# Optimization experiments

Measured on AMD Instinct MI355X. Metric: run time of the kernel, lower is better.

## Reference

```python
import jax, jax.numpy as jnp
import numpy as np

B = 16      # graphs
NPG = 1024  # nodes per graph (equal-sized, contiguous)
N = B * NPG
K = 12      # knn neighbors
DM = 128    # d_model
DH = 256    # d_hidden = 2*d_model
L = 3       # num_layers
DI = 2 * DM + 4  # msg mlp input dim


def _mlp2(x, W1, b1, W2, b2):
    return jax.nn.silu(x @ W1 + b1) @ W2 + b2


def setup_inputs() -> dict:
    key = jax.random.key(0)
    ks = list(jax.random.split(key, 16))
    def nrm(k, shape, fan):
        return jax.random.normal(k, shape, jnp.float32) / np.float32(np.sqrt(fan))
    return dict(
        x=jax.random.normal(ks[0], (N, 3), jnp.float32),
        batch=(jnp.arange(N) // NPG).astype(jnp.int32),
        in_W1=nrm(ks[1], (3, DM), 3), in_b1=jnp.zeros((DM,), jnp.float32),
        in_W2=nrm(ks[2], (DM, DM), DM), in_b2=jnp.zeros((DM,), jnp.float32),
        msg_W1=nrm(ks[3], (L, DI, DH), DI), msg_b1=jnp.zeros((L, DH), jnp.float32),
        msg_W2=nrm(ks[4], (L, DH, DM), DH), msg_b2=jnp.zeros((L, DM), jnp.float32),
        upd_W1=nrm(ks[5], (L, 2 * DM, DH), 2 * DM), upd_b1=jnp.zeros((L, DH), jnp.float32),
        upd_W2=nrm(ks[6], (L, DH, DM), DH), upd_b2=jnp.zeros((L, DM), jnp.float32),
        norm_w=jnp.ones((L, DM), jnp.float32), norm_b=jnp.zeros((L, DM), jnp.float32),
        norm_ms=jnp.ones((L, DM), jnp.float32),
        gate_W1=nrm(ks[7], (DM, DM), DM), gate_b1=jnp.zeros((DM,), jnp.float32),
        gate_W2=nrm(ks[8], (DM, 1), DM), gate_b2=jnp.zeros((1,), jnp.float32),
        head_W1=nrm(ks[9], (DM, DM), DM), head_b1=jnp.zeros((DM,), jnp.float32),
        head_W2=nrm(ks[10], (DM, 1), DM), head_b2=jnp.zeros((1,), jnp.float32),
    )


def _knn_edges(pos):
    # pos: [N,2]; graphs are contiguous blocks of NPG nodes -> blocked knn
    p3 = pos.reshape(B, NPG, 2)
    d2 = jnp.sum((p3[:, :, None, :] - p3[:, None, :, :]) ** 2, axis=-1)  # [B,n,n]
    d2 = jnp.where(jnp.eye(NPG, dtype=bool)[None], jnp.inf, d2)          # no self loops
    idx = jax.lax.top_k(-d2, K)[1]  # [B,n,K] nearest neighbors (sources)
    offs = (jnp.arange(B) * NPG)[:, None, None]
    src = (idx + offs).reshape(-1)
    dst = jnp.broadcast_to(jnp.arange(N).reshape(B, NPG, 1), (B, NPG, K)).reshape(-1)
    return src, dst


def _graph_norm(h, batch, cnt, w, b, ms):
    # PyG GraphNorm: out = w * (h - ms*mean) / sqrt(var + eps) + b, per-graph stats
    mean = jax.ops.segment_sum(h, batch, B) / cnt
    out = h - mean[batch] * ms
    var = jax.ops.segment_sum(out ** 2, batch, B) / cnt
    return w * out / jnp.sqrt(var + 1e-5)[batch] + b


def _forward(x, batch, in_W1, in_b1, in_W2, in_b2, msg_W1, msg_b1, msg_W2, msg_b2,
             upd_W1, upd_b1, upd_W2, upd_b2, norm_w, norm_b, norm_ms,
             gate_W1, gate_b1, gate_W2, gate_b2, head_W1, head_b1, head_W2, head_b2):
    pos = x[:, 1:3]
    src, dst = _knn_edges(pos)
    # edge_attr = [dx, dy, dist, ds]
    dp = pos[src] - pos[dst]
    dist = jnp.sqrt(jnp.sum(dp ** 2, axis=-1, keepdims=True) + 1e-12)
    ds = x[src, 0:1] - x[dst, 0:1]
    ea = jnp.concatenate([dp, dist, ds], axis=-1)  # [E,4]

    h = _mlp2(x, in_W1, in_b1, in_W2, in_b2)       # [N,DM]
    cnt = jax.ops.segment_sum(jnp.ones((N,), h.dtype), batch, B)[:, None]

    for i in range(L):
        m_in = jnp.concatenate([h[dst], h[src], ea], axis=-1)       # [E,2*DM+4]
        m = _mlp2(m_in, msg_W1[i], msg_b1[i], msg_W2[i], msg_b2[i])  # [E,DM]
        agg = jax.ops.segment_sum(m, dst, N)                         # scatter_add
        dh = _mlp2(jnp.concatenate([h, agg], axis=-1),
                   upd_W1[i], upd_b1[i], upd_W2[i], upd_b2[i])
        h = h + dh  # dropout is identity at inference
        h = _graph_norm(h, batch, cnt, norm_w[i], norm_b[i], norm_ms[i])

    # gated attention pool: segment softmax over gate logits
    gl = (jnp.tanh(h @ gate_W1 + gate_b1) @ gate_W2 + gate_b2)[:, 0]  # [N]
    gmax = jax.ops.segment_max(gl, batch, B)
    e = jnp.exp(gl - gmax[batch])
    a = e / jax.ops.segment_sum(e, batch, B)[batch]
    pooled = jax.ops.segment_sum(h * a[:, None], batch, B)            # [B,DM]

    return _mlp2(pooled, head_W1, head_b1, head_W2, head_b2)[:, 0]    # [B]


def reference(x, batch, in_W1, in_b1, in_W2, in_b2, msg_W1, msg_b1, msg_W2, msg_b2,
              upd_W1, upd_b1, upd_W2, upd_b2, norm_w, norm_b, norm_ms,
              gate_W1, gate_b1, gate_W2, gate_b2, head_W1, head_b1, head_W2, head_b2):
    return _forward(x, batch, in_W1, in_b1, in_W2, in_b2, msg_W1, msg_b1, msg_W2, msg_b2,
                    upd_W1, upd_b1, upd_W2, upd_b2, norm_w, norm_b, norm_ms,
                    gate_W1, gate_b1, gate_W2, gate_b2, head_W1, head_b1, head_W2, head_b2)
```

## Files before the change

### kernel.cpp

```cpp
#include <hip/hip_runtime.h>
#include <math.h>

#define NPTS 16384
#define BGR 16
#define NPGR 1024
#define KNN 12
#define DM 128
#define DH 256
#define NL 3
#define EDG (NPTS*KNN)

typedef unsigned short u16;
typedef unsigned int u32;
typedef __attribute__((ext_vector_type(8))) short short8;
typedef __attribute__((ext_vector_type(4))) float floatx4;

__device__ __forceinline__ float silu_f(float x) {
    return x / (1.0f + __expf(-x));
}
__device__ __forceinline__ u16 f2bf(float f) {
    union { float f; u32 u; } v; v.f = f;
    u32 r = v.u + 0x7fffu + ((v.u >> 16) & 1u);
    return (u16)(r >> 16);
}
__device__ __forceinline__ float bf2f(u16 b) {
    union { u32 u; float f; } v; v.u = ((u32)b) << 16;
    return v.f;
}

#define KPPB 16
#define PSTR 209
__global__ __launch_bounds__(256) void knn_kernel(const float* __restrict__ x,
                                                  int* __restrict__ srcb,
                                                  float* __restrict__ ea) {
#pragma clang fp contract(off)
    __shared__ float2 pxy[NPGR];
    __shared__ float s0[NPGR];
    __shared__ float sdf[KPPB * PSTR];
    __shared__ int   sif[KPPB * PSTR];
    __shared__ int   sel[KPPB][KNN];
    int t = threadIdx.x;
    int g   = blockIdx.x / (NPGR / KPPB);
    int blk = blockIdx.x % (NPGR / KPPB);
    int base = g * NPGR;
    for (int j = t; j < NPGR; j += 256) {
        const float* xp = x + (size_t)(base + j) * 3;
        s0[j] = xp[0];
        pxy[j] = make_float2(xp[1], xp[2]);
    }
    __syncthreads();
    int r  = t & 15;
    int pt = t >> 4;
    int il = blk * KPPB + pt;
    float2 pil = pxy[il];
    float xi = pil.x, yi = pil.y;
    float nd[KNN]; int ni[KNN];
#pragma unroll
    for (int k = 0; k < KNN; ++k) { nd[k] = 3.4e38f; ni[k] = 0x7fffffff; }
    for (int jj = 0; jj < 64; ++jj) {
        int j = jj * 16 + r;
        if (j == il) continue;
        float2 p = pxy[j];
        float dx = p.x - xi;
        float dy = p.y - yi;
        float dx2 = dx * dx;
        float dy2 = dy * dy;
        float d2 = dx2 + dy2;
        if (d2 < nd[KNN-1]) {
            float cd = d2; int ci = j;
#pragma unroll
            for (int k = 0; k < KNN; ++k) {
                bool sw = cd < nd[k];
                float tdv = sw ? nd[k] : cd;
                nd[k] = sw ? cd : nd[k];
                cd = tdv;
                int tiv = sw ? ni[k] : ci;
                ni[k] = sw ? ci : ni[k];
                ci = tiv;
            }
        }
    }
#pragma unroll
    for (int k = 0; k < KNN; ++k) {
        sdf[pt * PSTR + r * 13 + k] = nd[k];
        sif[pt * PSTR + r * 13 + k] = ni[k];
    }
    __syncthreads();
    if (r == 0) {
        int head[16];
#pragma unroll
        for (int q = 0; q < 16; ++q) head[q] = 0;
#pragma unroll
        for (int k = 0; k < KNN; ++k) {
            float bd = 3.4e38f; int bi = 0x7fffffff; int bq = 0;
#pragma unroll
            for (int q = 0; q < 16; ++q) {
                int hq = head[q];
                float d = (hq < KNN) ? sdf[pt * PSTR + q * 13 + hq] : 3.4e38f;
                int  ix = (hq < KNN) ? sif[pt * PSTR + q * 13 + hq] : 0x7fffffff;
                if (d < bd || (d == bd && ix < bi)) { bd = d; bi = ix; bq = q; }
            }
            head[bq]++;
            sel[pt][k] = bi;
        }
    }
    __syncthreads();
    if (r < KNN) {
        int k = r;
        int j = sel[pt][k];
        size_t e = (size_t)(base + il) * KNN + k;
        srcb[e] = base + j;
        float x0i = s0[il];
        float2 pj = pxy[j];
        float dpx = pj.x - xi, dpy = pj.y - yi;
        float a = dpx * dpx;
        float b = dpy * dpy;
        float dist = sqrtf(a + b + 1e-12f);
        float dsv = s0[j] - x0i;
        *(float4*)(ea + e * 4) = make_float4(dpx, dpy, dist, dsv);
    }
}

__global__ __launch_bounds__(128) void in_mlp_kernel(const float* __restrict__ x,
    const float* __restrict__ W1, const float* __restrict__ b1,
    const float* __restrict__ W2, const float* __restrict__ b2,
    float* __restrict__ h, u16* __restrict__ hh, u16* __restrict__ hl) {
    __shared__ float hid[8][DM];
    __shared__ float xl[8][3];
    int t = threadIdx.x;
    int nb = blockIdx.x * 8;
    if (t < 24) xl[t / 3][t % 3] = x[(size_t)nb * 3 + t];
    __syncthreads();
    float w0 = W1[t], w1 = W1[DM + t], w2 = W1[2 * DM + t], bb = b1[t];
#pragma unroll
    for (int gi = 0; gi < 8; ++gi) {
        float v = xl[gi][0] * w0 + xl[gi][1] * w1 + xl[gi][2] * w2 + bb;
        hid[gi][t] = silu_f(v);
    }
    __syncthreads();
    float acc[8];
    float b2v = b2[t];
#pragma unroll
    for (int gi = 0; gi < 8; ++gi) acc[gi] = b2v;
    for (int k = 0; k < DM; ++k) {
        float w = W2[k * DM + t];
#pragma unroll
        for (int gi = 0; gi < 8; ++gi) acc[gi] += hid[gi][k] * w;
    }
#pragma unroll
    for (int gi = 0; gi < 8; ++gi) {
        size_t idx = (size_t)(nb + gi) * DM + t;
        float v = acc[gi];
        h[idx] = v;
        u16 hi = f2bf(v);
        hh[idx] = hi;
        hl[idx] = f2bf(v - bf2f(hi));
    }
}

#define MBM 64
#define MBN 128
#define MBK 32
#define MLDA 40

__global__ __launch_bounds__(256) void mgemm_kernel(
    const u16* __restrict__ A0h, const u16* __restrict__ A0l, int k0, int lda0,
    const u16* __restrict__ A1h, const u16* __restrict__ A1l, int lda1,
    const u16* __restrict__ Wh, const u16* __restrict__ Wl, int K,
    const float* __restrict__ bias, int biasN,
    const float* __restrict__ resid, int ldres,
    float* __restrict__ outf, u16* __restrict__ outh, u16* __restrict__ outl, int ldout,
    int act)
{
    __shared__ __align__(16) u16 Ash[MBM * MLDA];
    __shared__ __align__(16) u16 Asl[MBM * MLDA];
    __shared__ __align__(16) u16 Bsh[MBN * MLDA];
    __shared__ __align__(16) u16 Bsl[MBN * MLDA];
    int t = threadIdx.x;
    int row0 = blockIdx.x * MBM, col0 = blockIdx.y * MBN;
    int lane = t & 63, w = t >> 6;
    int wm = (w >> 1) * 32, wn = (w & 1) * 64;
    int quad = lane >> 4, r15 = lane & 15;
    int arow = t >> 2, acol = (t & 3) * 8;
    int brow = t >> 1, bcol = (t & 1) * 16;

    floatx4 acc[2][4];
#pragma unroll
    for (int m = 0; m < 2; ++m)
#pragma unroll
        for (int n = 0; n < 4; ++n) acc[m][n] = (floatx4){0.f, 0.f, 0.f, 0.f};

    for (int kt = 0; kt < K; kt += MBK) {
        const u16 *Aph, *Apl;
        if (kt < k0) {
            Aph = A0h + (size_t)(row0 + arow) * lda0 + kt + acol;
            Apl = A0l + (size_t)(row0 + arow) * lda0 + kt + acol;
        } else {
            Aph = A1h + (size_t)(row0 + arow) * lda1 + (kt - k0) + acol;
            Apl = A1l + (size_t)(row0 + arow) * lda1 + (kt - k0) + acol;
        }
        uint4 avh = *(const uint4*)Aph;
        uint4 avl = *(const uint4*)Apl;
        const u16* Bph = Wh + (size_t)(col0 + brow) * K + kt + bcol;
        const u16* Bpl = Wl + (size_t)(col0 + brow) * K + kt + bcol;
        uint4 bh0 = ((const uint4*)Bph)[0];
        uint4 bh1 = ((const uint4*)Bph)[1];
        uint4 bl0 = ((const uint4*)Bpl)[0];
        uint4 bl1 = ((const uint4*)Bpl)[1];
        __syncthreads();
        *(uint4*)(Ash + arow * MLDA + acol) = avh;
        *(uint4*)(Asl + arow * MLDA + acol) = avl;
        uint4* bdh = (uint4*)(Bsh + brow * MLDA + bcol);
        uint4* bdl = (uint4*)(Bsl + brow * MLDA + bcol);
        bdh[0] = bh0; bdh[1] = bh1;
        bdl[0] = bl0; bdl[1] = bl1;
        __syncthreads();
        short8 ah[2], alo[2], bhf[4], blf[4];
#pragma unroll
        for (int m = 0; m < 2; ++m) {
            ah[m]  = *(const short8*)(Ash + (wm + m*16 + r15) * MLDA + quad*8);
            alo[m] = *(const short8*)(Asl + (wm + m*16 + r15) * MLDA + quad*8);
        }
#pragma unroll
        for (int n = 0; n < 4; ++n) {
            bhf[n] = *(const short8*)(Bsh + (wn + n*16 + r15) * MLDA + quad*8);
            blf[n] = *(const short8*)(Bsl + (wn + n*16 + r15) * MLDA + quad*8);
        }
#pragma unroll
        for (int m = 0; m < 2; ++m)
#pragma unroll
            for (int n = 0; n < 4; ++n) {
                acc[m][n] = __builtin_amdgcn_mfma_f32_16x16x32_bf16(ah[m],  bhf[n], acc[m][n], 0, 0, 0);
                acc[m][n] = __builtin_amdgcn_mfma_f32_16x16x32_bf16(ah[m],  blf[n], acc[m][n], 0, 0, 0);
                acc[m][n] = __builtin_amdgcn_mfma_f32_16x16x32_bf16(alo[m], bhf[n], acc[m][n], 0, 0, 0);
            }
    }
#pragma unroll
    for (int n = 0; n < 4; ++n) {
        int col = col0 + wn + n*16 + r15;
        float bv = (bias && col < biasN) ? bias[col] : 0.f;
#pragma unroll
        for (int m = 0; m < 2; ++m) {
#pragma unroll
            for (int reg = 0; reg < 4; ++reg) {
                int row = row0 + wm + m*16 + quad*4 + reg;
                float v = acc[m][n][reg] + bv;
                if (act == 1) v = silu_f(v);
                else if (act == 2) v = tanhf(v);
                if (resid) v += resid[(size_t)row * ldres + col];
                size_t oidx = (size_t)row * ldout + col;
                if (outf) outf[oidx] = v;
                if (outh) {
                    u16 hi = f2bf(v);
                    outh[oidx] = hi;
                    outl[oidx] = f2bf(v - bf2f(hi));
                }
            }
        }
    }
}

#define M2BM 128
__global__ __launch_bounds__(256) void mgemm128_kernel(
    const u16* __restrict__ A0h, const u16* __restrict__ A0l, int k0, int lda0,
    const u16* __restrict__ A1h, const u16* __restrict__ A1l, int lda1,
    const u16* __restrict__ Wh, const u16* __restrict__ Wl, int K,
    const float* __restrict__ bias, int biasN,
    float* __restrict__ outf, u16* __restrict__ outh, u16* __restrict__ outl, int ldout,
    int act)
{
    __shared__ __align__(16) u16 Ash[M2BM * MLDA];
    __shared__ __align__(16) u16 Asl[M2BM * MLDA];
    __shared__ __align__(16) u16 Bsh[MBN * MLDA];
    __shared__ __align__(16) u16 Bsl[MBN * MLDA];
    int t = threadIdx.x;
    int row0 = blockIdx.x * M2BM, col0 = blockIdx.y * MBN;
    int lane = t & 63, w = t >> 6;
    int wm = (w >> 1) * 64, wn = (w & 1) * 64;
    int quad = lane >> 4, r15 = lane & 15;
    int srow = t >> 1, scol = (t & 1) * 16;

    floatx4 acc[4][4];
#pragma unroll
    for (int m = 0; m < 4; ++m)
#pragma unroll
        for (int n = 0; n < 4; ++n) acc[m][n] = (floatx4){0.f, 0.f, 0.f, 0.f};

    for (int kt = 0; kt < K; kt += MBK) {
        const u16 *Aph, *Apl;
        if (kt < k0) {
            Aph = A0h + (size_t)(row0 + srow) * lda0 + kt + scol;
            Apl = A0l + (size_t)(row0 + srow) * lda0 + kt + scol;
        } else {
            Aph = A1h + (size_t)(row0 + srow) * lda1 + (kt - k0) + scol;
            Apl = A1l + (size_t)(row0 + srow) * lda1 + (kt - k0) + scol;
        }
        uint4 avh0 = ((const uint4*)Aph)[0];
        uint4 avh1 = ((const uint4*)Aph)[1];
        uint4 avl0 = ((const uint4*)Apl)[0];
        uint4 avl1 = ((const uint4*)Apl)[1];
        const u16* Bph = Wh + (size_t)(col0 + srow) * K + kt + scol;
        const u16* Bpl = Wl + (size_t)(col0 + srow) * K + kt + scol;
        uint4 bh0 = ((const uint4*)Bph)[0];
        uint4 bh1 = ((const uint4*)Bph)[1];
        uint4 bl0 = ((const uint4*)Bpl)[0];
        uint4 bl1 = ((const uint4*)Bpl)[1];
        __syncthreads();
        uint4* adh = (uint4*)(Ash + srow * MLDA + scol);
        uint4* adl = (uint4*)(Asl + srow * MLDA + scol);
        adh[0] = avh0; adh[1] = avh1;
        adl[0] = avl0; adl[1] = avl1;
        uint4* bdh = (uint4*)(Bsh + srow * MLDA + scol);
        uint4* bdl = (uint4*)(Bsl + srow * MLDA + scol);
        bdh[0] = bh0; bdh[1] = bh1;
        bdl[0] = bl0; bdl[1] = bl1;
        __syncthreads();
        short8 ah[4], alo[4], bhf[4], blf[4];
#pragma unroll
        for (int m = 0; m < 4; ++m) {
            ah[m]  = *(const short8*)(Ash + (wm + m*16 + r15) * MLDA + quad*8);
            alo[m] = *(const short8*)(Asl + (wm + m*16 + r15) * MLDA + quad*8);
        }
#pragma unroll
        for (int n = 0; n < 4; ++n) {
            bhf[n] = *(const short8*)(Bsh + (wn + n*16 + r15) * MLDA + quad*8);
            blf[n] = *(const short8*)(Bsl + (wn + n*16 + r15) * MLDA + quad*8);
        }
#pragma unroll
        for (int m = 0; m < 4; ++m)
#pragma unroll
            for (int n = 0; n < 4; ++n) {
                acc[m][n] = __builtin_amdgcn_mfma_f32_16x16x32_bf16(ah[m],  bhf[n], acc[m][n], 0, 0, 0);
                acc[m][n] = __builtin_amdgcn_mfma_f32_16x16x32_bf16(ah[m],  blf[n], acc[m][n], 0, 0, 0);
                acc[m][n] = __builtin_amdgcn_mfma_f32_16x16x32_bf16(alo[m], bhf[n], acc[m][n], 0, 0, 0);
            }
    }
#pragma unroll
    for (int n = 0; n < 4; ++n) {
        int col = col0 + wn + n*16 + r15;
        float bv = (bias && col < biasN) ? bias[col] : 0.f;
#pragma unroll
        for (int m = 0; m < 4; ++m) {
#pragma unroll
            for (int reg = 0; reg < 4; ++reg) {
                int row = row0 + wm + m*16 + quad*4 + reg;
                float v = acc[m][n][reg] + bv;
                if (act == 1) v = silu_f(v);
                size_t oidx = (size_t)row * ldout + col;
                if (outf) outf[oidx] = v;
                if (outh) {
                    u16 hi = f2bf(v);
                    outh[oidx] = hi;
                    outl[oidx] = f2bf(v - bf2f(hi));
                }
            }
        }
    }
}

__global__ __launch_bounds__(256) void edge_agg_kernel(
    const float* __restrict__ CS,
    const int* __restrict__ srcb, const float* __restrict__ ea,
    const float* __restrict__ W1ea,
    u16* __restrict__ HSh, u16* __restrict__ HSl)
{
    int i = blockIdx.x, t = threadIdx.x;
    __shared__ int ss[KNN];
    __shared__ float sea[KNN * 4];
    if (t < KNN) ss[t] = srcb[(size_t)i * KNN + t];
    if (t < KNN * 4) sea[t] = ea[(size_t)i * KNN * 4 + t];
    __syncthreads();
    float base = CS[(size_t)i * 512 + t];
    float wa = W1ea[t], wb = W1ea[DH + t], wc = W1ea[2 * DH + t], wd = W1ea[3 * DH + t];
    float hs = 0.f;
#pragma unroll
    for (int e = 0; e < KNN; ++e) {
        float v = base + CS[(size_t)ss[e] * 512 + 256 + t]
                + sea[e * 4 + 0] * wa + sea[e * 4 + 1] * wb
                + sea[e * 4 + 2] * wc + sea[e * 4 + 3] * wd;
        hs += silu_f(v);
    }
    size_t oidx = (size_t)i * DH + t;
    u16 hi = f2bf(hs);
    HSh[oidx] = hi;
    HSl[oidx] = f2bf(hs - bf2f(hi));
}

__global__ __launch_bounds__(256) void norm_part_kernel(const float* __restrict__ hn,
                                                        float* __restrict__ psum)
{
    int g = blockIdx.x, blk = blockIdx.y;
    int t = threadIdx.x, d = t & 127, half = t >> 7;
    size_t base = ((size_t)g * NPGR + (size_t)blk * 128 + half * 64) * DM;
    float s = 0.f, s2 = 0.f;
    for (int n = 0; n < 64; ++n) {
        float v = hn[base + (size_t)n * DM + d];
        s += v; s2 += v * v;
    }
    __shared__ float ps[2][DM], ps2[2][DM];
    ps[half][d] = s; ps2[half][d] = s2;
    __syncthreads();
    if (t < DM) {
        psum[(((size_t)g * 8 + blk) * 2 + 0) * DM + d] = ps[0][d] + ps[1][d];
        psum[(((size_t)g * 8 + blk) * 2 + 1) * DM + d] = ps2[0][d] + ps2[1][d];
    }
}

__global__ __launch_bounds__(256) void norm_apply_kernel(const float* __restrict__ hn,
    float* __restrict__ h, u16* __restrict__ hh, u16* __restrict__ hl,
    const float* __restrict__ psum,
    const float* __restrict__ w, const float* __restrict__ b, const float* __restrict__ ms)
{
    int g = blockIdx.x, blk = blockIdx.y, t = threadIdx.x;
    __shared__ float mmv[DM], rst[DM], wv[DM], bv[DM];
    if (t < DM) {
        float sum = 0.f, sq = 0.f;
        for (int q = 0; q < 8; ++q) {
            sum += psum[(((size_t)g * 8 + q) * 2 + 0) * DM + t];
            sq  += psum[(((size_t)g * 8 + q) * 2 + 1) * DM + t];
        }
        float mean = sum * (1.0f / NPGR);
        float mm = mean * ms[t];
        float var = sq * (1.0f / NPGR) - 2.f * mm * mean + mm * mm;
        mmv[t] = mm;
        rst[t] = 1.0f / sqrtf(var + 1e-5f);
        wv[t] = w[t]; bv[t] = b[t];
    }
    __syncthreads();
    size_t base = ((size_t)g * NPGR + (size_t)blk * 128) * DM;
    for (int i = t; i < 128 * DM; i += 256) {
        int dd = i & 127;
        float v = hn[base + i];
        float o = wv[dd] * (v - mmv[dd]) * rst[dd] + bv[dd];
        h[base + i] = o;
        u16 hi = f2bf(o);
        hh[base + i] = hi;
        hl[base + i] = f2bf(o - bf2f(hi));
    }
}

__global__ __launch_bounds__(256) void gate_dot_kernel(const float* __restrict__ Gh,
    const float* __restrict__ gW2, const float* __restrict__ gb2,
    float* __restrict__ gl)
{
    int t = threadIdx.x, lane = t & 63, w = t >> 6;
    int node = blockIdx.x * 4 + w;
    const float* gp = Gh + (size_t)node * DM;
    float v = gp[lane] * gW2[lane] + gp[lane + 64] * gW2[lane + 64];
    for (int off = 32; off > 0; off >>= 1) v += __shfl_down(v, off, 64);
    if (lane == 0) gl[node] = v + gb2[0];
}

__global__ __launch_bounds__(256) void pool_stats_kernel(const float* __restrict__ gl,
                                                         float* __restrict__ gstat)
{
    int g = blockIdx.x, t = threadIdx.x, lane = t & 63, w = t >> 6;
    __shared__ float red[4];
    const float* gp = gl + (size_t)g * NPGR;
    float mx = -3.4e38f;
    for (int n = t; n < NPGR; n += 256) mx = fmaxf(mx, gp[n]);
    for (int off = 32; off > 0; off >>= 1) mx = fmaxf(mx, __shfl_down(mx, off, 64));
    if (lane == 0) red[w] = mx;
    __syncthreads();
    float gmax = fmaxf(fmaxf(red[0], red[1]), fmaxf(red[2], red[3]));
    __syncthreads();
    float se = 0.f;
    for (int n = t; n < NPGR; n += 256) se += __expf(gp[n] - gmax);
    for (int off = 32; off > 0; off >>= 1) se += __shfl_down(se, off, 64);
    if (lane == 0) red[w] = se;
    __syncthreads();
    if (t == 0) { gstat[g * 2] = gmax; gstat[g * 2 + 1] = red[0] + red[1] + red[2] + red[3]; }
}

__global__ __launch_bounds__(256) void pool_part_kernel(const float* __restrict__ h,
    const float* __restrict__ gl, const float* __restrict__ gstat,
    float* __restrict__ ppool)
{
    int g = blockIdx.x, blk = blockIdx.y;
    int t = threadIdx.x, d = t & 127, half = t >> 7;
    float gmax = gstat[g * 2];
    size_t nbase = (size_t)g * NPGR + (size_t)blk * 128 + half * 64;
    float p = 0.f;
    for (int n = 0; n < 64; ++n)
        p += __expf(gl[nbase + n] - gmax) * h[(nbase + n) * DM + d];
    __shared__ float ps[2][DM];
    ps[half][d] = p;
    __syncthreads();
    if (t < DM) ppool[((size_t)g * 8 + blk) * DM + d] = ps[0][d] + ps[1][d];
}

__global__ __launch_bounds__(128) void pool_head_kernel(const float* __restrict__ ppool,
    const float* __restrict__ gstat,
    const float* __restrict__ hW1, const float* __restrict__ hb1,
    const float* __restrict__ hW2, const float* __restrict__ hb2,
    float* __restrict__ outp)
{
    int g = blockIdx.x, t = threadIdx.x;
    __shared__ float pl[DM];
    __shared__ float red[2];
    float ssum = gstat[g * 2 + 1];
    float p = 0.f;
    for (int q = 0; q < 8; ++q) p += ppool[((size_t)g * 8 + q) * DM + t];
    pl[t] = p / ssum;
    __syncthreads();
    float a = hb1[t];
    for (int k = 0; k < DM; ++k) a += pl[k] * hW1[k * DM + t];
    a = silu_f(a);
    float vv = a * hW2[t];
    int lane = t & 63, w = t >> 6;
    for (int off = 32; off > 0; off >>= 1) vv += __shfl_down(vv, off, 64);
    if (lane == 0) red[w] = vv;
    __syncthreads();
    if (t == 0) outp[g] = red[0] + red[1] + hb2[0];
}

__global__ __launch_bounds__(256) void precompute_kernel(
    const float* __restrict__ msgW2, const float* __restrict__ msgb2,
    const float* __restrict__ updW1, const float* __restrict__ updb1,
    float* __restrict__ W2U, float* __restrict__ bias2)
{
    int bid = blockIdx.x; int t = threadIdx.x;
    if (bid < NL * DH) {
        int l = bid / DH, k = bid % DH;
        const float* w2row = msgW2 + (size_t)l * DH * DM + (size_t)k * DM;
        const float* u1 = updW1 + (size_t)l * 2 * DM * DH;
        float acc = 0.f;
        for (int j = 0; j < DM; ++j) acc += w2row[j] * u1[(size_t)(DM + j) * DH + t];
        W2U[(size_t)l * DH * DH + (size_t)k * DH + t] = acc;
    } else {
        int l = bid - NL * DH;
        const float* u1 = updW1 + (size_t)l * 2 * DM * DH;
        const float* b2 = msgb2 + (size_t)l * DM;
        float acc = updb1[(size_t)l * DH + t];
        for (int j = 0; j < DM; ++j) acc += 12.0f * b2[j] * u1[(size_t)(DM + j) * DH + t];
        bias2[(size_t)l * DH + t] = acc;
    }
}

struct WJob { const float* src; u16* dh; u16* dl; int K, N, ldd, off; };
struct WJobs { WJob j[16]; };
__global__ __launch_bounds__(256) void wprep_kernel(WJobs jobs) {
    WJob jb = jobs.j[blockIdx.y];
    int n = blockIdx.x;
    if (n >= jb.N) return;
    for (int k = threadIdx.x; k < jb.K; k += 256) {
        float v = jb.src[(size_t)k * jb.N + n];
        u16 hi = f2bf(v);
        u16 lo = f2bf(v - bf2f(hi));
        jb.dh[(size_t)n * jb.ldd + jb.off + k] = hi;
        jb.dl[(size_t)n * jb.ldd + jb.off + k] = lo;
    }
}

extern "C" void kernel_launch(void* const* d_in, const int* in_sizes, int n_in,
                              void* d_out, int out_size, void* d_ws, size_t ws_size,
                              hipStream_t stream) {
    const float* x     = (const float*)d_in[0];
    const float* inW1  = (const float*)d_in[2];
    const float* inb1  = (const float*)d_in[3];
    const float* inW2  = (const float*)d_in[4];
    const float* inb2  = (const float*)d_in[5];
    const float* msgW1 = (const float*)d_in[6];
    const float* msgb1 = (const float*)d_in[7];
    const float* msgW2 = (const float*)d_in[8];
    const float* msgb2 = (const float*)d_in[9];
    const float* updW1 = (const float*)d_in[10];
    const float* updb1 = (const float*)d_in[11];
    const float* updW2 = (const float*)d_in[12];
    const float* updb2 = (const float*)d_in[13];
    const float* nw    = (const float*)d_in[14];
    const float* nb    = (const float*)d_in[15];
    const float* nms   = (const float*)d_in[16];
    const float* gW1   = (const float*)d_in[17];
    const float* gb1   = (const float*)d_in[18];
    const float* gW2   = (const float*)d_in[19];
    const float* gb2   = (const float*)d_in[20];
    const float* hW1   = (const float*)d_in[21];
    const float* hb1   = (const float*)d_in[22];
    const float* hW2   = (const float*)d_in[23];
    const float* hb2   = (const float*)d_in[24];
    float* outp = (float*)d_out;

    float* ws    = (float*)d_ws;
    float* h     = ws;
    float* CSb   = h + (size_t)NPTS * DM;
    float* hnb   = CSb + (size_t)NPTS * 512;
    float* W2U   = hnb + (size_t)NPTS * DM;
    float* bias2 = W2U + (size_t)NL * DH * DH;
    float* glb   = bias2 + NL * DH;
    int*   srcb  = (int*)(glb + NPTS);
    float* eab   = (float*)(srcb + EDG);
    float* psum  = eab + (size_t)EDG * 4;
    float* gstat = psum + 16 * 8 * 2 * DM;
    float* ppool = gstat + 32;
    u16* hh  = (u16*)(ppool + 16 * 8 * DM);
    u16* hl  = hh + (size_t)NPTS * DM;
    u16* HSh = hl + (size_t)NPTS * DM;
    u16* HSl = HSh + (size_t)NPTS * DH;
    u16* Th  = HSl + (size_t)NPTS * DH;
    u16* Tl  = Th + (size_t)NPTS * DH;
    u16* WCSh = Tl + (size_t)NPTS * DH;              u16* WCSl = WCSh + (size_t)NL * 512 * DM;
    u16* WTh = WCSl + (size_t)NL * 512 * DM;         u16* WTl = WTh + (size_t)NL * DH * 384;
    u16* WUh = WTl + (size_t)NL * DH * 384;          u16* WUl = WUh + (size_t)NL * DM * DH;
    u16* WGh = WUl + (size_t)NL * DM * DH;           u16* WGl = WGh + (size_t)DM * DM;

    hipLaunchKernelGGL(precompute_kernel, dim3(NL * DH + NL), dim3(DH), 0, stream,
                       msgW2, msgb2, updW1, updb1, W2U, bias2);

    WJobs jobs;
    int ji = 0;
    for (int l = 0; l < NL; ++l) {
        jobs.j[ji++] = WJob{ msgW1 + (size_t)l * 260 * DH,            WCSh + (size_t)l * 512 * DM,            WCSl + (size_t)l * 512 * DM,            128, 256, 128, 0 };
        jobs.j[ji++] = WJob{ msgW1 + (size_t)l * 260 * DH + 128 * DH, WCSh + (size_t)l * 512 * DM + 256 * DM, WCSl + (size_t)l * 512 * DM + 256 * DM, 128, 256, 128, 0 };
        jobs.j[ji++] = WJob{ updW1 + (size_t)l * 256 * DH,            WTh + (size_t)l * DH * 384, WTl + (size_t)l * DH * 384, 128, 256, 384, 0 };
        jobs.j[ji++] = WJob{ W2U   + (size_t)l * DH * DH,             WTh + (size_t)l * DH * 384, WTl + (size_t)l * DH * 384, 256, 256, 384, 128 };
        jobs.j[ji++] = WJob{ updW2 + (size_t)l * DH * DM,             WUh + (size_t)l * DM * DH, WUl + (size_t)l * DM * DH, 256, 128, 256, 0 };
    }
    jobs.j[ji++] = WJob{ gW1, WGh, WGl, 128, 128, 128, 0 };
    hipLaunchKernelGGL(wprep_kernel, dim3(256, 16), dim3(256), 0, stream, jobs);

    hipLaunchKernelGGL(knn_kernel, dim3(NPTS / KPPB), dim3(256), 0, stream, x, srcb, eab);
    hipLaunchKernelGGL(in_mlp_kernel, dim3(NPTS / 8), dim3(128), 0, stream,
                       x, inW1, inb1, inW2, inb2, h, hh, hl);

    for (int l = 0; l < NL; ++l) {
        const float* W1l = msgW1 + (size_t)l * 260 * DH;
        hipLaunchKernelGGL(mgemm128_kernel, dim3(NPTS / M2BM, 512 / MBN), dim3(256), 0, stream,
            hh, hl, DM, DM, (const u16*)nullptr, (const u16*)nullptr, 0,
            WCSh + (size_t)l * 512 * DM, WCSl + (size_t)l * 512 * DM, DM,
            msgb1 + (size_t)l * DH, 256,
            CSb, (u16*)nullptr, (u16*)nullptr, 512, 0);
        hipLaunchKernelGGL(edge_agg_kernel, dim3(NPTS), dim3(DH), 0, stream,
            CSb, srcb, eab, W1l + (size_t)2 * DM * DH, HSh, HSl);
        hipLaunchKernelGGL(mgemm128_kernel, dim3(NPTS / M2BM, DH / MBN), dim3(256), 0, stream,
            hh, hl, DM, DM, HSh, HSl, DH,
            WTh + (size_t)l * DH * 384, WTl + (size_t)l * DH * 384, 384,
            bias2 + (size_t)l * DH, DH,
            (float*)nullptr, Th, Tl, DH, 1);
        hipLaunchKernelGGL(mgemm_kernel, dim3(NPTS / MBM, DM / MBN), dim3(256), 0, stream,
            Th, Tl, DH, DH, (const u16*)nullptr, (const u16*)nullptr, 0,
            WUh + (size_t)l * DM * DH, WUl + (size_t)l * DM * DH, DH,
            updb2 + (size_t)l * DM, DM, h, DM,
            hnb, (u16*)nullptr, (u16*)nullptr, DM, 0);
        hipLaunchKernelGGL(norm_part_kernel, dim3(BGR, 8), dim3(256), 0, stream, hnb, psum);
        hipLaunchKernelGGL(norm_apply_kernel, dim3(BGR, 8), dim3(256), 0, stream,
            hnb, h, hh, hl, psum, nw + (size_t)l * DM, nb + (size_t)l * DM, nms + (size_t)l * DM);
    }

    hipLaunchKernelGGL(mgemm_kernel, dim3(NPTS / MBM, DM / MBN), dim3(256), 0, stream,
        hh, hl, DM, DM, (const u16*)nullptr, (const u16*)nullptr, 0,
        WGh, WGl, DM, gb1, DM, (const float*)nullptr, 0,
        hnb, (u16*)nullptr, (u16*)nullptr, DM, 2);
    hipLaunchKernelGGL(gate_dot_kernel, dim3(NPTS / 4), dim3(256), 0, stream,
        hnb, gW2, gb2, glb);

    hipLaunchKernelGGL(pool_stats_kernel, dim3(BGR), dim3(256), 0, stream, glb, gstat);
    hipLaunchKernelGGL(pool_part_kernel, dim3(BGR, 8), dim3(256), 0, stream, h, glb, gstat, ppool);
    hipLaunchKernelGGL(pool_head_kernel, dim3(BGR), dim3(128), 0, stream,
        ppool, gstat, hW1, hb1, hW2, hb2, outp);
}
```

Measured before the change: 566.4 us.

## Load GEMM tiles via direct global-to-LDS with XOR swizzle; retune knn split

Both bf16 split GEMM kernels now stage A and B tiles with global_load_lds (direct global-to-LDS DMA) instead of register round-trips. The padded LDS stride is replaced by an XOR-swizzled 32-wide layout to avoid bank conflicts. The knn kernel handles 32 points per block with 8 scanning threads per point instead of 16, which halves the merge width. One update GEMM switches from the 128-row to the 64-row tile variant, increasing the block count. Correctness of the swizzle and the implicit lane-to-LDS mapping of global_load_lds is a risk.

```diff
diff --git a/kernel.cpp b/kernel.cpp
--- a/kernel.cpp
+++ b/kernel.cpp
@@ -27,17 +27,24 @@
     union { u32 u; float f; } v; v.u = ((u32)b) << 16;
     return v.f;
 }
-
-#define KPPB 16
-#define PSTR 209
+__device__ __forceinline__ void glds16(const u16* gp, u16* lp) {
+    __builtin_amdgcn_global_load_lds(
+        (const __attribute__((address_space(1))) void*)gp,
+        (__attribute__((address_space(3))) void*)lp, 16, 0, 0);
+}
+__device__ __forceinline__ int lofs(int row, int q) {
+    return row * 32 + ((q ^ ((row >> 2) & 3)) << 3);
+}
+
+#define KPPB 32
 __global__ __launch_bounds__(256) void knn_kernel(const float* __restrict__ x,
                                                   int* __restrict__ srcb,
                                                   float* __restrict__ ea) {
 #pragma clang fp contract(off)
     __shared__ float2 pxy[NPGR];
     __shared__ float s0[NPGR];
-    __shared__ float sdf[KPPB * PSTR];
-    __shared__ int   sif[KPPB * PSTR];
+    __shared__ float sdf[256 * 13];
+    __shared__ int   sif[256 * 13];
     __shared__ int   sel[KPPB][KNN];
     int t = threadIdx.x;
     int g   = blockIdx.x / (NPGR / KPPB);
@@ -49,16 +56,16 @@
         pxy[j] = make_float2(xp[1], xp[2]);
     }
     __syncthreads();
-    int r  = t & 15;
-    int pt = t >> 4;
+    int r  = t & 7;
+    int pt = t >> 3;
     int il = blk * KPPB + pt;
     float2 pil = pxy[il];
     float xi = pil.x, yi = pil.y;
     float nd[KNN]; int ni[KNN];
 #pragma unroll
     for (int k = 0; k < KNN; ++k) { nd[k] = 3.4e38f; ni[k] = 0x7fffffff; }
-    for (int jj = 0; jj < 64; ++jj) {
-        int j = jj * 16 + r;
+    for (int jj = 0; jj < 128; ++jj) {
+        int j = jj * 8 + r;
         if (j == il) continue;
         float2 p = pxy[j];
         float dx = p.x - xi;
@@ -80,24 +87,25 @@
             }
         }
     }
+    int li = pt * 8 + r;
 #pragma unroll
     for (int k = 0; k < KNN; ++k) {
-        sdf[pt * PSTR + r * 13 + k] = nd[k];
-        sif[pt * PSTR + r * 13 + k] = ni[k];
+        sdf[li * 13 + k] = nd[k];
+        sif[li * 13 + k] = ni[k];
     }
     __syncthreads();
     if (r == 0) {
-        int head[16];
-#pragma unroll
-        for (int q = 0; q < 16; ++q) head[q] = 0;
+        int head[8];
+#pragma unroll
+        for (int q = 0; q < 8; ++q) head[q] = 0;
 #pragma unroll
         for (int k = 0; k < KNN; ++k) {
             float bd = 3.4e38f; int bi = 0x7fffffff; int bq = 0;
 #pragma unroll
-            for (int q = 0; q < 16; ++q) {
+            for (int q = 0; q < 8; ++q) {
                 int hq = head[q];
-                float d = (hq < KNN) ? sdf[pt * PSTR + q * 13 + hq] : 3.4e38f;
-                int  ix = (hq < KNN) ? sif[pt * PSTR + q * 13 + hq] : 0x7fffffff;
+                float d = (hq < KNN) ? sdf[(pt * 8 + q) * 13 + hq] : 3.4e38f;
+                int  ix = (hq < KNN) ? sif[(pt * 8 + q) * 13 + hq] : 0x7fffffff;
                 if (d < bd || (d == bd && ix < bi)) { bd = d; bi = ix; bq = q; }
             }
             head[bq]++;
@@ -105,12 +113,11 @@
         }
     }
     __syncthreads();
-    if (r < KNN) {
-        int k = r;
+    float x0i = s0[il];
+    for (int k = r; k < KNN; k += 8) {
         int j = sel[pt][k];
         size_t e = (size_t)(base + il) * KNN + k;
         srcb[e] = base + j;
-        float x0i = s0[il];
         float2 pj = pxy[j];
         float dpx = pj.x - xi, dpy = pj.y - yi;
         float a = dpx * dpx;
@@ -161,7 +168,6 @@
 #define MBM 64
 #define MBN 128
 #define MBK 32
-#define MLDA 40
 
 __global__ __launch_bounds__(256) void mgemm_kernel(
     const u16* __restrict__ A0h, const u16* __restrict__ A0l, int k0, int lda0,
@@ -172,17 +178,16 @@
     float* __restrict__ outf, u16* __restrict__ outh, u16* __restrict__ outl, int ldout,
     int act)
 {
-    __shared__ __align__(16) u16 Ash[MBM * MLDA];
-    __shared__ __align__(16) u16 Asl[MBM * MLDA];
-    __shared__ __align__(16) u16 Bsh[MBN * MLDA];
-    __shared__ __align__(16) u16 Bsl[MBN * MLDA];
+    __shared__ __align__(16) u16 Ash[MBM * 32];
+    __shared__ __align__(16) u16 Asl[MBM * 32];
+    __shared__ __align__(16) u16 Bsh[MBN * 32];
+    __shared__ __align__(16) u16 Bsl[MBN * 32];
     int t = threadIdx.x;
     int row0 = blockIdx.x * MBM, col0 = blockIdx.y * MBN;
     int lane = t & 63, w = t >> 6;
     int wm = (w >> 1) * 32, wn = (w & 1) * 64;
     int quad = lane >> 4, r15 = lane & 15;
-    int arow = t >> 2, acol = (t & 3) * 8;
-    int brow = t >> 1, bcol = (t & 1) * 16;
+    int rowl = lane >> 2, slot = lane & 3;
 
     floatx4 acc[2][4];
 #pragma unroll
@@ -191,40 +196,40 @@
         for (int n = 0; n < 4; ++n) acc[m][n] = (floatx4){0.f, 0.f, 0.f, 0.f};
 
     for (int kt = 0; kt < K; kt += MBK) {
-        const u16 *Aph, *Apl;
-        if (kt < k0) {
-            Aph = A0h + (size_t)(row0 + arow) * lda0 + kt + acol;
-            Apl = A0l + (size_t)(row0 + arow) * lda0 + kt + acol;
-        } else {
-            Aph = A1h + (size_t)(row0 + arow) * lda1 + (kt - k0) + acol;
-            Apl = A1l + (size_t)(row0 + arow) * lda1 + (kt - k0) + acol;
-        }
-        uint4 avh = *(const uint4*)Aph;
-        uint4 avl = *(const uint4*)Apl;
-        const u16* Bph = Wh + (size_t)(col0 + brow) * K + kt + bcol;
-        const u16* Bpl = Wl + (size_t)(col0 + brow) * K + kt + bcol;
-        uint4 bh0 = ((const uint4*)Bph)[0];
-        uint4 bh1 = ((const uint4*)Bph)[1];
-        uint4 bl0 = ((const uint4*)Bpl)[0];
-        uint4 bl1 = ((const uint4*)Bpl)[1];
+        const u16 *Abh, *Abl; int lda, ko;
+        if (kt < k0) { Abh = A0h; Abl = A0l; lda = lda0; ko = kt; }
+        else         { Abh = A1h; Abl = A1l; lda = lda1; ko = kt - k0; }
         __syncthreads();
-        *(uint4*)(Ash + arow * MLDA + acol) = avh;
-        *(uint4*)(Asl + arow * MLDA + acol) = avl;
-        uint4* bdh = (uint4*)(Bsh + brow * MLDA + bcol);
-        uint4* bdl = (uint4*)(Bsl + brow * MLDA + bcol);
-        bdh[0] = bh0; bdh[1] = bh1;
-        bdl[0] = bl0; bdl[1] = bl1;
+        {
+            int ra = w * 16 + rowl;
+            int gca = (slot ^ ((ra >> 2) & 3)) << 3;
+            size_t aoff = (size_t)(row0 + ra) * lda + ko + gca;
+            glds16(Abh + aoff, Ash + w * 16 * 32);
+            glds16(Abl + aoff, Asl + w * 16 * 32);
+            int rb0 = w * 32 + rowl;
+            int gc0 = (slot ^ ((rb0 >> 2) & 3)) << 3;
+            size_t boff0 = (size_t)(col0 + rb0) * K + kt + gc0;
+            glds16(Wh + boff0, Bsh + w * 32 * 32);
+            glds16(Wl + boff0, Bsl + w * 32 * 32);
+            int rb1 = rb0 + 16;
+            int gc1 = (slot ^ ((rb1 >> 2) & 3)) << 3;
+            size_t boff1 = (size_t)(col0 + rb1) * K + kt + gc1;
+            glds16(Wh + boff1, Bsh + (w * 32 + 16) * 32);
+            glds16(Wl + boff1, Bsl + (w * 32 + 16) * 32);
+        }
         __syncthreads();
         short8 ah[2], alo[2], bhf[4], blf[4];
 #pragma unroll
         for (int m = 0; m < 2; ++m) {
-            ah[m]  = *(const short8*)(Ash + (wm + m*16 + r15) * MLDA + quad*8);
-            alo[m] = *(const short8*)(Asl + (wm + m*16 + r15) * MLDA + quad*8);
+            int off = lofs(wm + m * 16 + r15, quad);
+            ah[m]  = *(const short8*)(Ash + off);
+            alo[m] = *(const short8*)(Asl + off);
         }
 #pragma unroll
         for (int n = 0; n < 4; ++n) {
-            bhf[n] = *(const short8*)(Bsh + (wn + n*16 + r15) * MLDA + quad*8);
-            blf[n] = *(const short8*)(Bsl + (wn + n*16 + r15) * MLDA + quad*8);
+            int off = lofs(wn + n * 16 + r15, quad);
+            bhf[n] = *(const short8*)(Bsh + off);
+            blf[n] = *(const short8*)(Bsl + off);
         }
 #pragma unroll
         for (int m = 0; m < 2; ++m)
@@ -269,16 +274,16 @@
     float* __restrict__ outf, u16* __restrict__ outh, u16* __restrict__ outl, int ldout,
     int act)
 {
-    __shared__ __align__(16) u16 Ash[M2BM * MLDA];
-    __shared__ __align__(16) u16 Asl[M2BM * MLDA];
-    __shared__ __align__(16) u16 Bsh[MBN * MLDA];
-    __shared__ __align__(16) u16 Bsl[MBN * MLDA];
+    __shared__ __align__(16) u16 Ash[M2BM * 32];
+    __shared__ __align__(16) u16 Asl[M2BM * 32];
+    __shared__ __align__(16) u16 Bsh[MBN * 32];
+    __shared__ __align__(16) u16 Bsl[MBN * 32];
     int t = threadIdx.x;
     int row0 = blockIdx.x * M2BM, col0 = blockIdx.y * MBN;
     int lane = t & 63, w = t >> 6;
     int wm = (w >> 1) * 64, wn = (w & 1) * 64;
     int quad = lane >> 4, r15 = lane & 15;
-    int srow = t >> 1, scol = (t & 1) * 16;
+    int rowl = lane >> 2, slot = lane & 3;
 
     floatx4 acc[4][4];
 #pragma unroll
@@ -287,44 +292,45 @@
         for (int n = 0; n < 4; ++n) acc[m][n] = (floatx4){0.f, 0.f, 0.f, 0.f};
 
     for (int kt = 0; kt < K; kt += MBK) {
-        const u16 *Aph, *Apl;
-        if (kt < k0) {
-            Aph = A0h + (size_t)(row0 + srow) * lda0 + kt + scol;
-            Apl = A0l + (size_t)(row0 + srow) * lda0 + kt + scol;
-        } else {
-            Aph = A1h + (size_t)(row0 + srow) * lda1 + (kt - k0) + scol;
-            Apl = A1l + (size_t)(row0 + srow) * lda1 + (kt - k0) + scol;
-        }
-        uint4 avh0 = ((const uint4*)Aph)[0];
-        uint4 avh1 = ((const uint4*)Aph)[1];
-        uint4 avl0 = ((const uint4*)Apl)[0];
-        uint4 avl1 = ((const uint4*)Apl)[1];
-        const u16* Bph = Wh + (size_t)(col0 + srow) * K + kt + scol;
-        const u16* Bpl = Wl + (size_t)(col0 + srow) * K + kt + scol;
-        uint4 bh0 = ((const uint4*)Bph)[0];
-        uint4 bh1 = ((const uint4*)Bph)[1];
-        uint4 bl0 = ((const uint4*)Bpl)[0];
-        uint4 bl1 = ((const uint4*)Bpl)[1];
+        const u16 *Abh, *Abl; int lda, ko;
+        if (kt < k0) { Abh = A0h; Abl = A0l; lda = lda0; ko = kt; }
+        else         { Abh = A1h; Abl = A1l; lda = lda1; ko = kt - k0; }
         __syncthreads();
-        uint4* adh = (uint4*)(Ash + srow * MLDA + scol);
-        uint4* adl = (uint4*)(Asl + srow * MLDA + scol);
-        adh[0] = avh0; adh[1] = avh1;
-        adl[0] = avl0; adl[1] = avl1;
-        uint4* bdh = (uint4*)(Bsh + srow * MLDA + scol);
-        uint4* bdl = (uint4*)(Bsl + srow * MLDA + scol);
-        bdh[0] = bh0; bdh[1] = bh1;
-        bdl[0] = bl0; bdl[1] = bl1;
+        {
+            int ra0 = w * 32 + rowl;
+            int gca0 = (slot ^ ((ra0 >> 2) & 3)) << 3;
+            size_t aoff0 = (size_t)(row0 + ra0) * lda + ko + gca0;
+            glds16(Abh + aoff0, Ash + w * 32 * 32);
+            glds16(Abl + aoff0, Asl + w * 32 * 32);
+            int ra1 = ra0 + 16;
+            int gca1 = (slot ^ ((ra1 >> 2) & 3)) << 3;
+            size_t aoff1 = (size_t)(row0 + ra1) * lda + ko + gca1;
+            glds16(Abh + aoff1, Ash + (w * 32 + 16) * 32);
+            glds16(Abl + aoff1, Asl + (w * 32 + 16) * 32);
+            int rb0 = w * 32 + rowl;
+            int gcb0 = (slot ^ ((rb0 >> 2) & 3)) << 3;
+            size_t boff0 = (size_t)(col0 + rb0) * K + kt + gcb0;
+            glds16(Wh + boff0, Bsh + w * 32 * 32);
+            glds16(Wl + boff0, Bsl + w * 32 * 32);
+            int rb1 = rb0 + 16;
+            int gcb1 = (slot ^ ((rb1 >> 2) & 3)) << 3;
+            size_t boff1 = (size_t)(col0 + rb1) * K + kt + gcb1;
+            glds16(Wh + boff1, Bsh + (w * 32 + 16) * 32);
+            glds16(Wl + boff1, Bsl + (w * 32 + 16) * 32);
+        }
         __syncthreads();
         short8 ah[4], alo[4], bhf[4], blf[4];
 #pragma unroll
         for (int m = 0; m < 4; ++m) {
-            ah[m]  = *(const short8*)(Ash + (wm + m*16 + r15) * MLDA + quad*8);
-            alo[m] = *(const short8*)(Asl + (wm + m*16 + r15) * MLDA + quad*8);
+            int off = lofs(wm + m * 16 + r15, quad);
+            ah[m]  = *(const short8*)(Ash + off);
+            alo[m] = *(const short8*)(Asl + off);
         }
 #pragma unroll
         for (int n = 0; n < 4; ++n) {
-            bhf[n] = *(const short8*)(Bsh + (wn + n*16 + r15) * MLDA + quad*8);
-            blf[n] = *(const short8*)(Bsl + (wn + n*16 + r15) * MLDA + quad*8);
+            int off = lofs(wn + n * 16 + r15, quad);
+            bhf[n] = *(const short8*)(Bsh + off);
+            blf[n] = *(const short8*)(Bsl + off);
         }
 #pragma unroll
         for (int m = 0; m < 4; ++m)
@@ -632,10 +638,10 @@
             CSb, (u16*)nullptr, (u16*)nullptr, 512, 0);
         hipLaunchKernelGGL(edge_agg_kernel, dim3(NPTS), dim3(DH), 0, stream,
             CSb, srcb, eab, W1l + (size_t)2 * DM * DH, HSh, HSl);
-        hipLaunchKernelGGL(mgemm128_kernel, dim3(NPTS / M2BM, DH / MBN), dim3(256), 0, stream,
+        hipLaunchKernelGGL(mgemm_kernel, dim3(NPTS / MBM, DH / MBN), dim3(256), 0, stream,
             hh, hl, DM, DM, HSh, HSl, DH,
             WTh + (size_t)l * DH * 384, WTl + (size_t)l * DH * 384, 384,
-            bias2 + (size_t)l * DH, DH,
+            bias2 + (size_t)l * DH, DH, (const float*)nullptr, 0,
             (float*)nullptr, Th, Tl, DH, 1);
         hipLaunchKernelGGL(mgemm_kernel, dim3(NPTS / MBM, DM / MBN), dim3(256), 0, stream,
             Th, Tl, DH, DH, (const u16*)nullptr, (const u16*)nullptr, 0,
```

Result: faster. 539.5 us (-4.8%).
